# Kernel optimization log

Hardware: AMD Instinct MI355X
Metric: run time of the kernel (lower is better)

## Reference

```python
import jax, jax.numpy as jnp
import numpy as np

N_NODES = 49984   # 32 graphs x 1562 nodes
N_EDGES = 799744  # avg degree 16
DIM_IN = 64
WIDTH = 256
DEPTH = 3         # depth+1 = 4 GCNConv blocks
N_GRAPHS = 32
NODES_PER_GRAPH = 1562


def setup_inputs() -> dict:
    key = jax.random.key(0)
    ks = jax.random.split(key, 12)
    nb = DEPTH + 1
    s_f = 1.0 / np.sqrt(DIM_IN)
    s_g = 1.0 / np.sqrt(WIDTH)
    return {
        "x": jax.random.normal(ks[0], (N_NODES, DIM_IN), dtype=jnp.float32),
        "edge_index": jax.random.randint(ks[1], (2, N_EDGES), 0, N_NODES, dtype=jnp.int32),
        "center": jax.random.randint(ks[2], (N_GRAPHS,), 0, NODES_PER_GRAPH, dtype=jnp.int32),
        "ptr": jnp.arange(N_GRAPHS + 1, dtype=jnp.int32) * NODES_PER_GRAPH,
        # foot: Conv1d(dim_input, width, 1) == per-node linear
        "Wf": jax.random.uniform(ks[3], (WIDTH, DIM_IN), jnp.float32, -s_f, s_f),
        "bf": jax.random.uniform(ks[4], (WIDTH,), jnp.float32, -s_f, s_f),
        # stacked GCNConv params: weight [nb, width, width] (in->out), bias [nb, width]
        "Wg": jax.random.uniform(ks[5], (nb, WIDTH, WIDTH), jnp.float32, -s_g, s_g),
        "bg": jax.random.uniform(ks[6], (nb, WIDTH), jnp.float32, -s_g, s_g),
        # head: Conv1d(width, 7, 1)
        "Wh": jax.random.uniform(ks[7], (7, WIDTH), jnp.float32, -s_g, s_g),
        "bh": jax.random.uniform(ks[8], (7,), jnp.float32, -s_g, s_g),
    }


def reference(x, edge_index, center, ptr, Wf, bf, Wg, bg, Wh, bh):
    N = x.shape[0]
    # foot: 1x1 conv (per-node linear) + exact GELU; dropout = identity (eval)
    h = jax.nn.gelu(x @ Wf.T + bf, approximate=False)  # [N, W]

    # gcn_norm with self-loops (same for every layer since edges are static)
    loops = jnp.arange(N, dtype=edge_index.dtype)
    row = jnp.concatenate([edge_index[0], loops])  # source
    col = jnp.concatenate([edge_index[1], loops])  # target
    deg = jax.ops.segment_sum(jnp.ones_like(row, dtype=h.dtype), col, num_segments=N)
    dis = jnp.where(deg > 0, jax.lax.rsqrt(jnp.maximum(deg, 1.0)), 0.0)
    norm = dis[row] * dis[col]  # [E+N]

    for l in range(Wg.shape[0]):
        xl = h @ Wg[l]                                   # [N, W] linear transform
        msg = xl[row] * norm[:, None]                    # gather + edge scale
        agg = jax.ops.segment_sum(msg, col, num_segments=N) + bg[l]
        h = h + agg                                      # residual

    out = jax.nn.gelu(h, approximate=False) @ Wh.T + bh  # [N, 7]
    return out[center + ptr[:-1]]                        # [B, 7]
```

## Files before the change

### kernel.cpp

```cpp
#include <hip/hip_runtime.h>
#include <math.h>

#define WIDTH 256
typedef unsigned short u16;
typedef unsigned int u32;
typedef __attribute__((ext_vector_type(4))) float f32x4;
typedef __attribute__((ext_vector_type(8))) short bf16x8;

__device__ __forceinline__ float gelu_exact(float v) {
    return 0.5f * v * (1.0f + erff(v * 0.70710678118654752f));
}
__device__ __forceinline__ u16 f2b(float x) {
    u32 u = __builtin_bit_cast(u32, x);
    return (u16)((u + 0x7fffu + ((u >> 16) & 1u)) >> 16);
}
__device__ __forceinline__ float b2f_lo(u32 v) {
    return __builtin_bit_cast(float, v << 16);
}
__device__ __forceinline__ float b2f_hi(u32 v) {
    return __builtin_bit_cast(float, v & 0xffff0000u);
}
__device__ __forceinline__ float b2fu(u16 b) {
    return __builtin_bit_cast(float, ((u32)b) << 16);
}
__device__ __forceinline__ u32 pack2(float a, float b) {
    return (u32)f2b(a) | ((u32)f2b(b) << 16);
}

#define PREP_WG   (4 * 65536)
#define PREP_WF   (256 * 64)
__global__ void k_prep(const float* __restrict__ Wg, const float* __restrict__ Wf,
                       const float* __restrict__ x,
                       u16* __restrict__ WgT, u16* __restrict__ WfT,
                       u16* __restrict__ xb, int total8) {
    int idx = blockIdx.x * blockDim.x + threadIdx.x;
    if (idx < PREP_WG) {
        int l = idx >> 16;
        int k = (idx >> 8) & 255;
        int n = idx & 255;
        WgT[(size_t)l * 65536 + (size_t)n * 256 + k] = f2b(Wg[idx]);
    } else if (idx < PREP_WG + PREP_WF) {
        int j = idx - PREP_WG;
        WfT[j] = f2b(Wf[j]);
    } else if (idx < PREP_WG + PREP_WF + total8) {
        int i = idx - (PREP_WG + PREP_WF);
        const float4 v0 = *reinterpret_cast<const float4*>(&x[(size_t)i * 8]);
        const float4 v1 = *reinterpret_cast<const float4*>(&x[(size_t)i * 8 + 4]);
        uint4 o;
        o.x = pack2(v0.x, v0.y);
        o.y = pack2(v0.z, v0.w);
        o.z = pack2(v1.x, v1.y);
        o.w = pack2(v1.z, v1.w);
        *reinterpret_cast<uint4*>(&xb[(size_t)i * 8]) = o;
    }
}

__global__ void k_hist8(const int* __restrict__ col, int* __restrict__ deg8,
                        u16* __restrict__ rank, int E, int N) {
    int i = blockIdx.x * blockDim.x + threadIdx.x;
    if (i < E) {
        const int c = blockIdx.x & 7;
        rank[i] = (u16)atomicAdd(&deg8[(size_t)c * N + col[i]], 1);
    }
}

__global__ __launch_bounds__(256) void k_scan1(const int* __restrict__ deg8, int* __restrict__ off,
                                               int* __restrict__ part, float* __restrict__ dis,
                                               u16* __restrict__ base8, int N) {
    __shared__ int buf[256];
    const int t = threadIdx.x;
    const int gid = blockIdx.x * 256 + t;
    int d = 0;
    if (gid < N) {
        int run = 0;
#pragma unroll
        for (int c = 0; c < 8; ++c) {
            base8[(size_t)c * N + gid] = (u16)run;
            run += deg8[(size_t)c * N + gid];
        }
        d = run;
        dis[gid] = rsqrtf(1.0f + (float)run);
    }
    buf[t] = d;
    __syncthreads();
#pragma unroll
    for (int dd = 1; dd < 256; dd <<= 1) {
        int add = (t >= dd) ? buf[t - dd] : 0;
        __syncthreads();
        buf[t] += add;
        __syncthreads();
    }
    if (gid < N) off[gid] = buf[t] - d;
    if (t == 255) part[blockIdx.x] = buf[255];
}

__global__ __launch_bounds__(256) void k_scan3(int* __restrict__ off, const int* __restrict__ part,
                                               int NB, int N, int E) {
    __shared__ int buf[256];
    const int t = threadIdx.x;
    int v = (t < NB) ? part[t] : 0;
    buf[t] = v;
    __syncthreads();
#pragma unroll
    for (int d = 1; d < 256; d <<= 1) {
        int add = (t >= d) ? buf[t - d] : 0;
        __syncthreads();
        buf[t] += add;
        __syncthreads();
    }
    const int base = (blockIdx.x == 0) ? 0 : buf[blockIdx.x - 1];
    const int gid = blockIdx.x * 256 + t;
    if (gid < N) off[gid] += base;
    if (gid == 0) off[N] = E;
}

__global__ void k_fill(const int* __restrict__ row, const int* __restrict__ col,
                       const u16* __restrict__ rank, const u16* __restrict__ base8,
                       const float* __restrict__ dis,
                       const int* __restrict__ off, u32* __restrict__ csr, int E, int N) {
    int i = blockIdx.x * blockDim.x + threadIdx.x;
    if (i < E) {
        const int c = blockIdx.x & 7;
        const int r = row[i];
        const int cc = col[i];
        const int pos = off[cc] + (int)base8[(size_t)c * N + cc] + (int)rank[i];
        csr[pos] = (u32)(u16)r | ((u32)f2b(dis[r]) << 16);
    }
}

__global__ void k_front(const int* __restrict__ center, const int* __restrict__ ptr,
                        const int* __restrict__ off, const u32* __restrict__ csr,
                        int* __restrict__ flags, int* __restrict__ list, int* __restrict__ cnt) {
    const int g = blockIdx.x;
    const int node = center[g] + ptr[g];
    const int t = threadIdx.x;
    const int e0 = off[node];
    const int e1 = off[node + 1];
    if (t == 0) {
        if (atomicExch(&flags[node], 1) == 0) list[atomicAdd(cnt, 1)] = node;
    }
    for (int e = e0 + t; e < e1; e += 256) {
        const int s = (int)(csr[e] & 0xffffu);
        if (atomicExch(&flags[s], 1) == 0) list[atomicAdd(cnt, 1)] = s;
    }
}

__global__ void k_front2(const int* __restrict__ off, const u32* __restrict__ csr,
                         const int* __restrict__ list1, const int* __restrict__ cnt1,
                         int* __restrict__ flags2, int* __restrict__ list2, int* __restrict__ cnt2) {
    const int n1 = cnt1[0];
    const int t = threadIdx.x;
    for (int idx = blockIdx.x; idx < n1; idx += gridDim.x) {
        const int node = list1[idx];
        if (t == 0) {
            if (atomicExch(&flags2[node], 1) == 0) list2[atomicAdd(cnt2, 1)] = node;
        }
        const int e0 = off[node];
        const int e1 = off[node + 1];
        for (int e = e0 + t; e < e1; e += 256) {
            const int s = (int)(csr[e] & 0xffffu);
            if (atomicExch(&flags2[s], 1) == 0) list2[atomicAdd(cnt2, 1)] = s;
        }
    }
}

template <int KDIM, bool FOOT>
__global__ __launch_bounds__(512) void k_gemm_mfma(const u16* __restrict__ A,
                                                   const u16* __restrict__ BT,
                                                   const float* __restrict__ bias,
                                                   u16* __restrict__ Cb,
                                                   float* __restrict__ Cf, int nrows) {
    __shared__ u16 As[128 * 64];
    __shared__ u16 Bs[256 * 64];

    const int tid = threadIdx.x;
    const int w = tid >> 6;
    const int l = tid & 63;
    const int m0 = blockIdx.x * 128;
    const int wr = w >> 2;
    const int wc = w & 3;

    const int lr = l >> 3;
    const int lc = l & 7;
    const int src_slot = lc ^ lr;

    f32x4 acc[4][4] = {};

#pragma unroll
    for (int ks = 0; ks < KDIM / 64; ++ks) {
        const int k0 = ks * 64;
#pragma unroll
        for (int i = 0; i < 2; ++i) {
            const u16* asrc = A + (size_t)(m0 + 16 * w + 8 * i + lr) * KDIM + k0 + src_slot * 8;
            __builtin_amdgcn_global_load_lds(
                (const __attribute__((address_space(1))) u32*)asrc,
                (__attribute__((address_space(3))) u32*)(As + (16 * w + 8 * i) * 64), 16, 0, 0);
        }
#pragma unroll
        for (int j = 0; j < 4; ++j) {
            const u16* bsrc = BT + (size_t)(32 * w + 8 * j + lr) * KDIM + k0 + src_slot * 8;
            __builtin_amdgcn_global_load_lds(
                (const __attribute__((address_space(1))) u32*)bsrc,
                (__attribute__((address_space(3))) u32*)(Bs + (32 * w + 8 * j) * 64), 16, 0, 0);
        }
        asm volatile("s_waitcnt vmcnt(0)" ::: "memory");
        __syncthreads();

        bf16x8 a[4][2], b[4][2];
#pragma unroll
        for (int fr = 0; fr < 4; ++fr) {
            const int row = 64 * wr + fr * 16 + (l & 15);
#pragma unroll
            for (int kk = 0; kk < 2; ++kk)
                a[fr][kk] = *reinterpret_cast<const bf16x8*>(
                    &As[row * 64 + ((kk * 4 + (l >> 4)) ^ (row & 7)) * 8]);
        }
#pragma unroll
        for (int fc = 0; fc < 4; ++fc) {
            const int row = 64 * wc + fc * 16 + (l & 15);
#pragma unroll
            for (int kk = 0; kk < 2; ++kk)
                b[fc][kk] = *reinterpret_cast<const bf16x8*>(
                    &Bs[row * 64 + ((kk * 4 + (l >> 4)) ^ (row & 7)) * 8]);
        }
#pragma unroll
        for (int fr = 0; fr < 4; ++fr)
#pragma unroll
            for (int fc = 0; fc < 4; ++fc) {
                acc[fr][fc] = __builtin_amdgcn_mfma_f32_16x16x32_bf16(a[fr][0], b[fc][0], acc[fr][fc], 0, 0, 0);
                acc[fr][fc] = __builtin_amdgcn_mfma_f32_16x16x32_bf16(a[fr][1], b[fc][1], acc[fr][fc], 0, 0, 0);
            }
        __syncthreads();
    }

    const int r0 = (l >> 4) * 4;
    const int ci = l & 15;
#pragma unroll
    for (int fr = 0; fr < 4; ++fr)
#pragma unroll
        for (int fc = 0; fc < 4; ++fc) {
            const int col = 64 * wc + fc * 16 + ci;
#pragma unroll
            for (int r = 0; r < 4; ++r) {
                const int row = m0 + 64 * wr + fr * 16 + r0 + r;
                if (row < nrows) {
                    const size_t p = (size_t)row * WIDTH + col;
                    if (FOOT) {
                        const float o = gelu_exact(acc[fr][fc][r] + bias[col]);
                        Cf[p] = o;
                        Cb[p] = f2b(o);
                    } else {
                        Cb[p] = f2b(acc[fr][fc][r]);
                    }
                }
            }
        }
}

__global__ __launch_bounds__(512) void k_gemm_gather(const u16* __restrict__ A,
                                                     const u16* __restrict__ BT,
                                                     u16* __restrict__ Cb,
                                                     const int* __restrict__ list,
                                                     const int* __restrict__ cnt) {
    __shared__ u16 As[128 * 64];
    __shared__ u16 Bs[256 * 64];

    const int nrows = cnt[0];
    const int tid = threadIdx.x;
    const int w = tid >> 6;
    const int l = tid & 63;
    const int wr = w >> 2;
    const int wc = w & 3;

    const int lr = l >> 3;
    const int lc = l & 7;
    const int src_slot = lc ^ lr;

    for (int m0 = blockIdx.x * 128; m0 < nrows; m0 += gridDim.x * 128) {
        f32x4 acc[4][4] = {};

#pragma unroll
        for (int ks = 0; ks < 4; ++ks) {
            const int k0 = ks * 64;
#pragma unroll
            for (int i = 0; i < 2; ++i) {
                int ridx = m0 + 16 * w + 8 * i + lr;
                ridx = min(ridx, nrows - 1);
                const u16* asrc = A + (size_t)list[ridx] * WIDTH + k0 + src_slot * 8;
                __builtin_amdgcn_global_load_lds(
                    (const __attribute__((address_space(1))) u32*)asrc,
                    (__attribute__((address_space(3))) u32*)(As + (16 * w + 8 * i) * 64), 16, 0, 0);
            }
#pragma unroll
            for (int j = 0; j < 4; ++j) {
                const u16* bsrc = BT + (size_t)(32 * w + 8 * j + lr) * WIDTH + k0 + src_slot * 8;
                __builtin_amdgcn_global_load_lds(
                    (const __attribute__((address_space(1))) u32*)bsrc,
                    (__attribute__((address_space(3))) u32*)(Bs + (32 * w + 8 * j) * 64), 16, 0, 0);
            }
            asm volatile("s_waitcnt vmcnt(0)" ::: "memory");
            __syncthreads();

            bf16x8 a[4][2], b[4][2];
#pragma unroll
            for (int fr = 0; fr < 4; ++fr) {
                const int row = 64 * wr + fr * 16 + (l & 15);
#pragma unroll
                for (int kk = 0; kk < 2; ++kk)
                    a[fr][kk] = *reinterpret_cast<const bf16x8*>(
                        &As[row * 64 + ((kk * 4 + (l >> 4)) ^ (row & 7)) * 8]);
            }
#pragma unroll
            for (int fc = 0; fc < 4; ++fc) {
                const int row = 64 * wc + fc * 16 + (l & 15);
#pragma unroll
                for (int kk = 0; kk < 2; ++kk)
                    b[fc][kk] = *reinterpret_cast<const bf16x8*>(
                        &Bs[row * 64 + ((kk * 4 + (l >> 4)) ^ (row & 7)) * 8]);
            }
#pragma unroll
            for (int fr = 0; fr < 4; ++fr)
#pragma unroll
                for (int fc = 0; fc < 4; ++fc) {
                    acc[fr][fc] = __builtin_amdgcn_mfma_f32_16x16x32_bf16(a[fr][0], b[fc][0], acc[fr][fc], 0, 0, 0);
                    acc[fr][fc] = __builtin_amdgcn_mfma_f32_16x16x32_bf16(a[fr][1], b[fc][1], acc[fr][fc], 0, 0, 0);
                }
            __syncthreads();
        }

        const int r0 = (l >> 4) * 4;
        const int ci = l & 15;
#pragma unroll
        for (int fr = 0; fr < 4; ++fr)
#pragma unroll
            for (int fc = 0; fc < 4; ++fc) {
                const int col = 64 * wc + fc * 16 + ci;
#pragma unroll
                for (int r = 0; r < 4; ++r) {
                    const int row = m0 + 64 * wr + fr * 16 + r0 + r;
                    if (row < nrows)
                        Cb[(size_t)list[row] * WIDTH + col] = f2b(acc[fr][fc][r]);
                }
            }
    }
}

#define EDGE_FMA(vv, dd_)                          \
    acc[0] = fmaf(dd_, b2f_lo(vv.x), acc[0]);      \
    acc[1] = fmaf(dd_, b2f_hi(vv.x), acc[1]);      \
    acc[2] = fmaf(dd_, b2f_lo(vv.y), acc[2]);      \
    acc[3] = fmaf(dd_, b2f_hi(vv.y), acc[3]);

__device__ __forceinline__ void agg_node_body(const int* __restrict__ off,
                                              const u32* __restrict__ csr,
                                              const float* __restrict__ dis,
                                              const u16* __restrict__ xlb,
                                              const float* __restrict__ bg,
                                              float* __restrict__ h,
                                              u16* __restrict__ hb,
                                              int node, int hl, int ch0) {
    const int c = ch0 + hl * 4;
    const int e0 = off[node];
    const int e1 = off[node + 1];
    const float di = dis[node];

    float acc[4];
    {
        const uint2 v = *reinterpret_cast<const uint2*>(&xlb[(size_t)node * WIDTH + c]);
        acc[0] = di * b2f_lo(v.x);
        acc[1] = di * b2f_hi(v.x);
        acc[2] = di * b2f_lo(v.y);
        acc[3] = di * b2f_hi(v.y);
    }

    for (int base = e0; base < e1; base += 32) {
        const int m = min(32, e1 - base);
        u32 ep = 0;
        if (hl < m) ep = csr[base + hl];
        int j = 0;
        for (; j + 8 <= m; j += 8) {
            uint2 vv[8];
            float dd[8];
#pragma unroll
            for (int q = 0; q < 8; ++q) {
                const u32 e = (u32)__shfl((int)ep, j + q, 32);
                dd[q] = b2f_hi(e);
                vv[q] = *reinterpret_cast<const uint2*>(&xlb[(size_t)(e & 0xffffu) * WIDTH + c]);
            }
#pragma unroll
            for (int q = 0; q < 8; ++q) { EDGE_FMA(vv[q], dd[q]) }
        }
        if (j + 4 <= m) {
            uint2 vv[4];
            float dd[4];
#pragma unroll
            for (int q = 0; q < 4; ++q) {
                const u32 e = (u32)__shfl((int)ep, j + q, 32);
                dd[q] = b2f_hi(e);
                vv[q] = *reinterpret_cast<const uint2*>(&xlb[(size_t)(e & 0xffffu) * WIDTH + c]);
            }
#pragma unroll
            for (int q = 0; q < 4; ++q) { EDGE_FMA(vv[q], dd[q]) }
            j += 4;
        }
        for (; j < m; ++j) {
            const u32 e = (u32)__shfl((int)ep, j, 32);
            const float dj = b2f_hi(e);
            const uint2 v = *reinterpret_cast<const uint2*>(&xlb[(size_t)(e & 0xffffu) * WIDTH + c]);
            EDGE_FMA(v, dj)
        }
    }

    const size_t p = (size_t)node * WIDTH + c;
    const float4 hv = *reinterpret_cast<const float4*>(&h[p]);
    const float4 bv = *reinterpret_cast<const float4*>(&bg[c]);
    const float o0 = hv.x + bv.x + di * acc[0];
    const float o1 = hv.y + bv.y + di * acc[1];
    const float o2 = hv.z + bv.z + di * acc[2];
    const float o3 = hv.w + bv.w + di * acc[3];
    float4 w0;
    w0.x = o0; w0.y = o1; w0.z = o2; w0.w = o3;
    *reinterpret_cast<float4*>(&h[p]) = w0;
    uint2 ob;
    ob.x = pack2(o0, o1);
    ob.y = pack2(o2, o3);
    *reinterpret_cast<uint2*>(&hb[p]) = ob;
}

__global__ __launch_bounds__(256) void k_agg(const int* __restrict__ off,
                                             const u32* __restrict__ csr,
                                             const float* __restrict__ dis,
                                             const u16* __restrict__ xlb,
                                             const float* __restrict__ bg,
                                             float* __restrict__ h,
                                             u16* __restrict__ hb, int nbh, int N) {
    int bh = blockIdx.x;
    int ch0 = 0;
    if (bh >= nbh) { ch0 = 128; bh -= nbh; }
    const int node = (bh * 256 + threadIdx.x) >> 5;
    if (node >= N) return;
    agg_node_body(off, csr, dis, xlb, bg, h, hb, node, threadIdx.x & 31, ch0);
}

__global__ __launch_bounds__(256) void k_agg_list(const int* __restrict__ off,
                                                  const u32* __restrict__ csr,
                                                  const float* __restrict__ dis,
                                                  const u16* __restrict__ xlb,
                                                  const float* __restrict__ bg,
                                                  float* __restrict__ h,
                                                  u16* __restrict__ hb,
                                                  const int* __restrict__ list,
                                                  const int* __restrict__ cnt) {
    const int nitems = cnt[0] * 2;
    const int hl = threadIdx.x & 31;
    const int stride = (gridDim.x * 256) >> 5;
    for (int item = (blockIdx.x * 256 + threadIdx.x) >> 5; item < nitems; item += stride) {
        const int node = list[item >> 1];
        const int ch0 = (item & 1) << 7;
        agg_node_body(off, csr, dis, xlb, bg, h, hb, node, hl, ch0);
    }
}
#undef EDGE_FMA

__global__ __launch_bounds__(256) void k_tail(const int* __restrict__ off,
                                              const u32* __restrict__ csr,
                                              const float* __restrict__ dis,
                                              const u16* __restrict__ hb,
                                              const float* __restrict__ h,
                                              const float* __restrict__ Wg3,
                                              const float* __restrict__ bg3,
                                              const float* __restrict__ Wh,
                                              const float* __restrict__ bh,
                                              const int* __restrict__ center,
                                              const int* __restrict__ ptr,
                                              float* __restrict__ out) {
    __shared__ float aggK[256];
    __shared__ u32 es[256];
    __shared__ float gs[256];
    const int g = blockIdx.x;
    const int t = threadIdx.x;
    const int node = center[g] + ptr[g];
    const int e0 = off[node];
    const int e1 = off[node + 1];
    const float di = dis[node];

    float acc = di * b2fu(hb[(size_t)node * WIDTH + t]);
    for (int base = e0; base < e1; base += 256) {
        const int m = min(256, e1 - base);
        if (t < m) es[t] = csr[base + t];
        __syncthreads();
        int j = 0;
        for (; j + 4 <= m; j += 4) {
            const u32 a0 = es[j + 0], a1 = es[j + 1], a2 = es[j + 2], a3 = es[j + 3];
            const float v0 = b2fu(hb[(size_t)(a0 & 0xffffu) * WIDTH + t]);
            const float v1 = b2fu(hb[(size_t)(a1 & 0xffffu) * WIDTH + t]);
            const float v2 = b2fu(hb[(size_t)(a2 & 0xffffu) * WIDTH + t]);
            const float v3 = b2fu(hb[(size_t)(a3 & 0xffffu) * WIDTH + t]);
            acc = fmaf(b2f_hi(a0), v0, acc);
            acc = fmaf(b2f_hi(a1), v1, acc);
            acc = fmaf(b2f_hi(a2), v2, acc);
            acc = fmaf(b2f_hi(a3), v3, acc);
        }
        for (; j < m; ++j) {
            const u32 a = es[j];
            acc = fmaf(b2f_hi(a), b2fu(hb[(size_t)(a & 0xffffu) * WIDTH + t]), acc);
        }
        __syncthreads();
    }
    aggK[t] = acc;
    __syncthreads();

    float mv = 0.0f;
#pragma unroll 8
    for (int k = 0; k < 256; ++k)
        mv = fmaf(aggK[k], Wg3[(size_t)k * 256 + t], mv);
    const float h4 = h[(size_t)node * WIDTH + t] + bg3[t] + di * mv;
    gs[t] = gelu_exact(h4);
    __syncthreads();
    if (t < 7) {
        float o = bh[t];
        for (int k = 0; k < 256; ++k)
            o = fmaf(gs[k], Wh[t * 256 + k], o);
        out[g * 7 + t] = o;
    }
}

extern "C" void kernel_launch(void* const* d_in, const int* in_sizes, int n_in,
                              void* d_out, int out_size, void* d_ws, size_t ws_size,
                              hipStream_t stream) {
    const float* x      = (const float*)d_in[0];
    const int*   ei     = (const int*)d_in[1];
    const int*   center = (const int*)d_in[2];
    const int*   ptr    = (const int*)d_in[3];
    const float* Wf     = (const float*)d_in[4];
    const float* bf     = (const float*)d_in[5];
    const float* Wg     = (const float*)d_in[6];
    const float* bg     = (const float*)d_in[7];
    const float* Wh     = (const float*)d_in[8];
    const float* bh     = (const float*)d_in[9];

    const int E = in_sizes[1] / 2;
    const int N = in_sizes[0] / 64;
    const int B = in_sizes[2];

    char* ws = (char*)d_ws;
    size_t o = 0;
    float* h       = (float*)(ws + o); o += (size_t)N * WIDTH * 4;
    u16*   hb      = (u16*)  (ws + o); o += (size_t)N * WIDTH * 2;
    u16*   xlb     = (u16*)  (ws + o); o += (size_t)N * WIDTH * 2;
    u16*   xb      = (u16*)  (ws + o); o += (size_t)N * 64 * 2;
    float* dis     = (float*)(ws + o); o += (size_t)N * 4;
    int*   deg8    = (int*)  (ws + o); o += (size_t)N * 8 * 4;
    u16*   base8   = (u16*)  (ws + o); o += (size_t)N * 8 * 2;
    int*   off     = (int*)  (ws + o); o += (size_t)(N + 1) * 4;
    int*   part    = (int*)  (ws + o); o += 1024;
    u16*   rank    = (u16*)  (ws + o); o += (size_t)E * 2;
    u32*   csr     = (u32*)  (ws + o); o += (size_t)E * 4;
    u16*   WgT     = (u16*)  (ws + o); o += (size_t)4 * 65536 * 2;
    u16*   WfT     = (u16*)  (ws + o); o += (size_t)256 * 64 * 2;
    int*   flags   = (int*)  (ws + o); o += (size_t)N * 4;
    int*   flags2  = (int*)  (ws + o); o += (size_t)N * 4;
    int*   cnt     = (int*)  (ws + o); o += 128;
    int*   cnt2    = (int*)  (ws + o); o += 128;
    int*   list1   = (int*)  (ws + o); o += (size_t)N * 4;
    int*   list2   = (int*)  (ws + o); o += (size_t)N * 4;

    const int* rowv = ei;
    const int* colv = ei + E;

    const int nb = (N + 255) / 256;
    const int eb = (E + 255) / 256;

    hipMemsetAsync(deg8, 0, (size_t)N * 8 * 4, stream);
    hipMemsetAsync(flags, 0, (size_t)N * 8 + 256, stream);
    const int total8 = N * 64 / 8;
    const int prep_threads = PREP_WG + PREP_WF + total8;
    k_prep<<<(prep_threads + 255) / 256, 256, 0, stream>>>(Wg, Wf, x, WgT, WfT, xb, total8);
    k_hist8<<<eb, 256, 0, stream>>>(colv, deg8, rank, E, N);
    k_scan1<<<nb, 256, 0, stream>>>(deg8, off, part, dis, base8, N);
    k_scan3<<<nb, 256, 0, stream>>>(off, part, nb, N, E);
    k_fill<<<eb, 256, 0, stream>>>(rowv, colv, rank, base8, dis, off, csr, E, N);
    k_front<<<B, 256, 0, stream>>>(center, ptr, off, csr, flags, list1, cnt);
    k_front2<<<64, 256, 0, stream>>>(off, csr, list1, cnt, flags2, list2, cnt2);

    const int gb = (N + 127) / 128;
    k_gemm_mfma<64, true><<<gb, 512, 0, stream>>>(xb, WfT, bf, hb, h, N);

    const int nbh = N / 8;
    k_gemm_mfma<256, false><<<gb, 512, 0, stream>>>(hb, WgT, nullptr, xlb, nullptr, N);
    k_agg<<<2 * nbh, 256, 0, stream>>>(off, csr, dis, xlb, bg, h, hb, nbh, N);

    k_gemm_mfma<256, false><<<gb, 512, 0, stream>>>(hb, WgT + (size_t)1 * 65536, nullptr, xlb, nullptr, N);
    k_agg_list<<<1024, 256, 0, stream>>>(off, csr, dis, xlb, bg + (size_t)1 * WIDTH, h, hb, list2, cnt2);

    k_gemm_gather<<<128, 512, 0, stream>>>(hb, WgT + (size_t)2 * 65536, xlb, list2, cnt2);
    k_agg_list<<<256, 256, 0, stream>>>(off, csr, dis, xlb, bg + (size_t)2 * WIDTH, h, hb, list1, cnt);

    k_tail<<<B, 256, 0, stream>>>(off, csr, dis, hb, h,
                                  Wg + (size_t)3 * 65536, bg + (size_t)3 * WIDTH,
                                  Wh, bh, center, ptr, (float*)d_out);
}
```

Baseline: 274.9 us.

## Skip fp32 residual writes for unneeded nodes and widen list-aggregation lanes

Adds a per-node flag so aggregation kernels store the fp32 residual h only for nodes whose fp32 value is read by later layers; the bf16 copy is always written. The frontier-list aggregation now uses 16-lane groups, each lane handling 8 channels with 16-byte gathers, to increase bytes per memory request. This cuts global write traffic in the full-graph layer and reduces the number of instructions per gathered row. It relies on the frontier flags correctly marking every node whose fp32 state is needed downstream.

```diff
diff --git a/kernel.cpp b/kernel.cpp
--- a/kernel.cpp
+++ b/kernel.cpp
@@ -358,6 +358,7 @@
                                               const float* __restrict__ bg,
                                               float* __restrict__ h,
                                               u16* __restrict__ hb,
+                                              const int* __restrict__ wflags,
                                               int node, int hl, int ch0) {
     const int c = ch0 + hl * 4;
     const int e0 = off[node];
@@ -418,14 +419,118 @@
     const float o1 = hv.y + bv.y + di * acc[1];
     const float o2 = hv.z + bv.z + di * acc[2];
     const float o3 = hv.w + bv.w + di * acc[3];
-    float4 w0;
-    w0.x = o0; w0.y = o1; w0.z = o2; w0.w = o3;
-    *reinterpret_cast<float4*>(&h[p]) = w0;
+    if (wflags == nullptr || wflags[node]) {
+        float4 w0;
+        w0.x = o0; w0.y = o1; w0.z = o2; w0.w = o3;
+        *reinterpret_cast<float4*>(&h[p]) = w0;
+    }
     uint2 ob;
     ob.x = pack2(o0, o1);
     ob.y = pack2(o2, o3);
     *reinterpret_cast<uint2*>(&hb[p]) = ob;
 }
+#undef EDGE_FMA
+
+#define EDGE_FMA16(vv, dd_)                        \
+    acc[0] = fmaf(dd_, b2f_lo(vv.x), acc[0]);      \
+    acc[1] = fmaf(dd_, b2f_hi(vv.x), acc[1]);      \
+    acc[2] = fmaf(dd_, b2f_lo(vv.y), acc[2]);      \
+    acc[3] = fmaf(dd_, b2f_hi(vv.y), acc[3]);      \
+    acc[4] = fmaf(dd_, b2f_lo(vv.z), acc[4]);      \
+    acc[5] = fmaf(dd_, b2f_hi(vv.z), acc[5]);      \
+    acc[6] = fmaf(dd_, b2f_lo(vv.w), acc[6]);      \
+    acc[7] = fmaf(dd_, b2f_hi(vv.w), acc[7]);
+
+__device__ __forceinline__ void agg_node_body16(const int* __restrict__ off,
+                                                const u32* __restrict__ csr,
+                                                const float* __restrict__ dis,
+                                                const u16* __restrict__ xlb,
+                                                const float* __restrict__ bg,
+                                                float* __restrict__ h,
+                                                u16* __restrict__ hb,
+                                                const int* __restrict__ wflags,
+                                                int node, int hl, int ch0) {
+    const int c = ch0 + hl * 8;
+    const int e0 = off[node];
+    const int e1 = off[node + 1];
+    const float di = dis[node];
+
+    float acc[8];
+    {
+        const uint4 v = *reinterpret_cast<const uint4*>(&xlb[(size_t)node * WIDTH + c]);
+        acc[0] = di * b2f_lo(v.x); acc[1] = di * b2f_hi(v.x);
+        acc[2] = di * b2f_lo(v.y); acc[3] = di * b2f_hi(v.y);
+        acc[4] = di * b2f_lo(v.z); acc[5] = di * b2f_hi(v.z);
+        acc[6] = di * b2f_lo(v.w); acc[7] = di * b2f_hi(v.w);
+    }
+
+    for (int base = e0; base < e1; base += 16) {
+        const int m = min(16, e1 - base);
+        u32 ep = 0;
+        if (hl < m) ep = csr[base + hl];
+        int j = 0;
+        for (; j + 8 <= m; j += 8) {
+            uint4 vv[8];
+            float dd[8];
+#pragma unroll
+            for (int q = 0; q < 8; ++q) {
+                const u32 e = (u32)__shfl((int)ep, j + q, 16);
+                dd[q] = b2f_hi(e);
+                vv[q] = *reinterpret_cast<const uint4*>(&xlb[(size_t)(e & 0xffffu) * WIDTH + c]);
+            }
+#pragma unroll
+            for (int q = 0; q < 8; ++q) { EDGE_FMA16(vv[q], dd[q]) }
+        }
+        if (j + 4 <= m) {
+            uint4 vv[4];
+            float dd[4];
+#pragma unroll
+            for (int q = 0; q < 4; ++q) {
+                const u32 e = (u32)__shfl((int)ep, j + q, 16);
+                dd[q] = b2f_hi(e);
+                vv[q] = *reinterpret_cast<const uint4*>(&xlb[(size_t)(e & 0xffffu) * WIDTH + c]);
+            }
+#pragma unroll
+            for (int q = 0; q < 4; ++q) { EDGE_FMA16(vv[q], dd[q]) }
+            j += 4;
+        }
+        for (; j < m; ++j) {
+            const u32 e = (u32)__shfl((int)ep, j, 16);
+            const float dj = b2f_hi(e);
+            const uint4 v = *reinterpret_cast<const uint4*>(&xlb[(size_t)(e & 0xffffu) * WIDTH + c]);
+            EDGE_FMA16(v, dj)
+        }
+    }
+
+    const size_t p = (size_t)node * WIDTH + c;
+    const float4 h0 = *reinterpret_cast<const float4*>(&h[p]);
+    const float4 h1 = *reinterpret_cast<const float4*>(&h[p + 4]);
+    const float4 b0 = *reinterpret_cast<const float4*>(&bg[c]);
+    const float4 b1 = *reinterpret_cast<const float4*>(&bg[c + 4]);
+    float o[8];
+    o[0] = h0.x + b0.x + di * acc[0];
+    o[1] = h0.y + b0.y + di * acc[1];
+    o[2] = h0.z + b0.z + di * acc[2];
+    o[3] = h0.w + b0.w + di * acc[3];
+    o[4] = h1.x + b1.x + di * acc[4];
+    o[5] = h1.y + b1.y + di * acc[5];
+    o[6] = h1.z + b1.z + di * acc[6];
+    o[7] = h1.w + b1.w + di * acc[7];
+    if (wflags == nullptr || wflags[node]) {
+        float4 w0, w1;
+        w0.x = o[0]; w0.y = o[1]; w0.z = o[2]; w0.w = o[3];
+        w1.x = o[4]; w1.y = o[5]; w1.z = o[6]; w1.w = o[7];
+        *reinterpret_cast<float4*>(&h[p]) = w0;
+        *reinterpret_cast<float4*>(&h[p + 4]) = w1;
+    }
+    uint4 ob;
+    ob.x = pack2(o[0], o[1]);
+    ob.y = pack2(o[2], o[3]);
+    ob.z = pack2(o[4], o[5]);
+    ob.w = pack2(o[6], o[7]);
+    *reinterpret_cast<uint4*>(&hb[p]) = ob;
+}
+#undef EDGE_FMA16
 
 __global__ __launch_bounds__(256) void k_agg(const int* __restrict__ off,
                                              const u32* __restrict__ csr,
@@ -433,13 +538,15 @@
                                              const u16* __restrict__ xlb,
                                              const float* __restrict__ bg,
                                              float* __restrict__ h,
-                                             u16* __restrict__ hb, int nbh, int N) {
+                                             u16* __restrict__ hb,
+                                             const int* __restrict__ flags2,
+                                             int nbh, int N) {
     int bh = blockIdx.x;
     int ch0 = 0;
     if (bh >= nbh) { ch0 = 128; bh -= nbh; }
     const int node = (bh * 256 + threadIdx.x) >> 5;
     if (node >= N) return;
-    agg_node_body(off, csr, dis, xlb, bg, h, hb, node, threadIdx.x & 31, ch0);
+    agg_node_body(off, csr, dis, xlb, bg, h, hb, flags2, node, threadIdx.x & 31, ch0);
 }
 
 __global__ __launch_bounds__(256) void k_agg_list(const int* __restrict__ off,
@@ -450,17 +557,17 @@
                                                   float* __restrict__ h,
                                                   u16* __restrict__ hb,
                                                   const int* __restrict__ list,
-                                                  const int* __restrict__ cnt) {
+                                                  const int* __restrict__ cnt,
+                                                  const int* __restrict__ wflags) {
     const int nitems = cnt[0] * 2;
-    const int hl = threadIdx.x & 31;
-    const int stride = (gridDim.x * 256) >> 5;
-    for (int item = (blockIdx.x * 256 + threadIdx.x) >> 5; item < nitems; item += stride) {
+    const int hl = threadIdx.x & 15;
+    const int stride = (gridDim.x * 256) >> 4;
+    for (int item = (blockIdx.x * 256 + threadIdx.x) >> 4; item < nitems; item += stride) {
         const int node = list[item >> 1];
         const int ch0 = (item & 1) << 7;
-        agg_node_body(off, csr, dis, xlb, bg, h, hb, node, hl, ch0);
-    }
-}
-#undef EDGE_FMA
+        agg_node_body16(off, csr, dis, xlb, bg, h, hb, wflags, node, hl, ch0);
+    }
+}
 
 __global__ __launch_bounds__(256) void k_tail(const int* __restrict__ off,
                                               const u32* __restrict__ csr,
@@ -588,13 +695,13 @@
 
     const int nbh = N / 8;
     k_gemm_mfma<256, false><<<gb, 512, 0, stream>>>(hb, WgT, nullptr, xlb, nullptr, N);
-    k_agg<<<2 * nbh, 256, 0, stream>>>(off, csr, dis, xlb, bg, h, hb, nbh, N);
+    k_agg<<<2 * nbh, 256, 0, stream>>>(off, csr, dis, xlb, bg, h, hb, flags2, nbh, N);
 
     k_gemm_mfma<256, false><<<gb, 512, 0, stream>>>(hb, WgT + (size_t)1 * 65536, nullptr, xlb, nullptr, N);
-    k_agg_list<<<1024, 256, 0, stream>>>(off, csr, dis, xlb, bg + (size_t)1 * WIDTH, h, hb, list2, cnt2);
+    k_agg_list<<<1024, 256, 0, stream>>>(off, csr, dis, xlb, bg + (size_t)1 * WIDTH, h, hb, list2, cnt2, flags);
 
     k_gemm_gather<<<128, 512, 0, stream>>>(hb, WgT + (size_t)2 * 65536, xlb, list2, cnt2);
-    k_agg_list<<<256, 256, 0, stream>>>(off, csr, dis, xlb, bg + (size_t)2 * WIDTH, h, hb, list1, cnt);
+    k_agg_list<<<256, 256, 0, stream>>>(off, csr, dis, xlb, bg + (size_t)2 * WIDTH, h, hb, list1, cnt, nullptr);
 
     k_tail<<<B, 256, 0, stream>>>(off, csr, dis, hb, h,
                                   Wg + (size_t)3 * 65536, bg + (size_t)3 * WIDTH,
```

Measured after the change: 272.4 us. About the same (-0.9%).
